# Performance work log

Measured on AMD Instinct MI355X. Metric: run time of the kernel, lower is better.

Reference implementation:

```python
import jax, jax.numpy as jnp
import numpy as np

B, C, T = 2, 128, 25000
OUT_C = 128
N_NODES = B * T            # 50000, nodes after flatten
N_EDGES = 800000           # avg degree 16


def setup_inputs() -> dict:
    key = jax.random.key(0)
    k1, k2, k3 = jax.random.split(key, 3)
    x = jax.random.normal(k1, (B, C, T), dtype=jnp.float32)
    W = jax.random.normal(k2, (C, OUT_C), dtype=jnp.float32) * (1.0 / np.sqrt(C))
    bias = jnp.zeros((OUT_C,), dtype=jnp.float32)
    edge_index = jax.random.randint(k3, (2, N_EDGES), 0, N_NODES, dtype=jnp.int64)
    return {"x": x, "W": W, "bias": bias, "edge_index": edge_index}


def reference(x, W, bias, edge_index):
    b, c, t = x.shape
    n = b * t
    flat = x.transpose(0, 2, 1).reshape(n, c)          # [N, C]
    h = flat @ W                                       # [N, OUT_C] transform first (GCNConv)
    src, dst = edge_index[0], edge_index[1]
    # in-degree with self-loops (PyG GCNConv default symmetric norm)
    deg = jnp.zeros((n,), dtype=h.dtype).at[dst].add(1.0) + 1.0
    dinv_sqrt = jax.lax.rsqrt(deg)
    norm = dinv_sqrt[src] * dinv_sqrt[dst]             # [E]
    msgs = h[src] * norm[:, None]                      # [E, OUT_C] gather + scale
    agg = jax.ops.segment_sum(msgs, dst, num_segments=n)
    agg = agg + h * (1.0 / deg)[:, None]               # self-loop term: norm_ii = 1/deg_i
    out = jax.nn.relu(agg + bias)
    return out.reshape(b, t, -1).transpose(0, 2, 1)    # [B, OUT_C, T]
```

## Files before the change

kernel.cpp:

```cpp
#include <hip/hip_runtime.h>

#define TT 25000
#define BB 2
#define CC 128
#define NN (BB*TT)
#define NB ((NN + 255) / 256)

typedef __attribute__((ext_vector_type(8))) short bf16x8;
typedef __attribute__((ext_vector_type(4))) float f32x4;

__device__ inline unsigned short f2bf(float f) {
    unsigned int u = __float_as_uint(f);
    u += 0x7FFF + ((u >> 16) & 1);
    return (unsigned short)(u >> 16);
}
__device__ inline float bfhi(unsigned int v) { return __uint_as_float(v << 16); }
__device__ inline float bflo(unsigned int v) { return __uint_as_float(v & 0xFFFF0000u); }

__global__ __launch_bounds__(256) void k_deg(const int* __restrict__ dst, int E,
                                             int* __restrict__ deg,
                                             int* __restrict__ eseq) {
    int base = blockIdx.x * 1024 + threadIdx.x;
    int d[4]; bool ok[4];
#pragma unroll
    for (int u = 0; u < 4; ++u) {
        int i = base + u * 256;
        ok[u] = (i < E);
        d[u] = ok[u] ? dst[i] : 0;
    }
#pragma unroll
    for (int u = 0; u < 4; ++u)
        if (ok[u]) eseq[base + u * 256] = atomicAdd(&deg[d[u]], 1);
}

__global__ __launch_bounds__(256) void k_bsum(const int* __restrict__ deg,
                                              int* __restrict__ bsum) {
    __shared__ int red[256];
    int tid = threadIdx.x;
    int i = blockIdx.x * 256 + tid;
    red[tid] = (i < NN) ? deg[i] : 0;
    __syncthreads();
#pragma unroll
    for (int o = 128; o > 0; o >>= 1) {
        if (tid < o) red[tid] += red[tid + o];
        __syncthreads();
    }
    if (tid == 0) bsum[blockIdx.x] = red[0];
}

__global__ __launch_bounds__(256) void k_scan2(const int* __restrict__ deg,
                                               const int* __restrict__ bsum,
                                               int* __restrict__ off,
                                               float* __restrict__ dinv) {
    __shared__ int part[256];
    __shared__ int bpref;
    int tid = threadIdx.x;
    int i = blockIdx.x * 256 + tid;

    part[tid] = (tid < NB && tid < blockIdx.x) ? bsum[tid] : 0;
    __syncthreads();
#pragma unroll
    for (int o = 128; o > 0; o >>= 1) {
        if (tid < o) part[tid] += part[tid + o];
        __syncthreads();
    }
    if (tid == 0) bpref = part[0];
    __syncthreads();
    int base = bpref;
    __syncthreads();

    int v = (i < NN) ? deg[i] : 0;
    part[tid] = v;
    __syncthreads();
#pragma unroll
    for (int o = 1; o < 256; o <<= 1) {
        int u = (tid >= o) ? part[tid - o] : 0;
        __syncthreads();
        part[tid] += u;
        __syncthreads();
    }
    int incl = part[tid];
    if (i < NN) {
        off[i]  = base + incl - v;
        dinv[i] = rsqrtf((float)(v + 1));
    }
    if (i == NN - 1) off[NN] = base + incl;
}

__global__ __launch_bounds__(256) void k_fill(const int* __restrict__ src,
                                              const int* __restrict__ dst, int E,
                                              const int* __restrict__ off,
                                              const int* __restrict__ eseq,
                                              int* __restrict__ csr_src) {
    int i = blockIdx.x * blockDim.x + threadIdx.x;
    if (i < E) {
        int d = dst[i];
        csr_src[off[d] + eseq[i]] = src[i];
    }
}

__global__ __launch_bounds__(256) void k_gemm(const float* __restrict__ x,
                                              const float* __restrict__ W,
                                              const float* __restrict__ dinv,
                                              unsigned short* __restrict__ h) {
    __shared__ __align__(16) unsigned short a_lds[4][4][64][8];
    __shared__ __align__(16) unsigned short b_lds[8][4][64][8];
    int tid = threadIdx.x;
    int n0 = blockIdx.x * 64;

    {
        int m = tid & 63;
        int n = n0 + m;
        bool ok = (n < NN);
        int b = 0, t = 0;
        if (ok) { b = n / TT; t = n - b * TT; }
        const float* xp = x + ((size_t)b * CC) * TT + t;
        int mt = m >> 4, lm = m & 15;
#pragma unroll
        for (int p = 0; p < 4; ++p) {
            int kg = (tid >> 6) + p * 4;
            unsigned short tmp[8];
#pragma unroll
            for (int j = 0; j < 8; ++j) {
                float v = ok ? xp[(size_t)(kg * 8 + j) * TT] : 0.f;
                tmp[j] = f2bf(v);
            }
            int kk = kg >> 2, q = kg & 3;
            *(bf16x8*)&a_lds[mt][kk][lm | (q << 4)][0] = *(bf16x8*)tmp;
        }
    }
    {
        int nc = tid & 127;
        int nt = nc >> 4, ln = nc & 15;
#pragma unroll
        for (int p = 0; p < 8; ++p) {
            int kg = (tid >> 7) + p * 2;
            unsigned short tmp[8];
#pragma unroll
            for (int j = 0; j < 8; ++j)
                tmp[j] = f2bf(W[(kg * 8 + j) * CC + nc]);
            int kk = kg >> 2, q = kg & 3;
            *(bf16x8*)&b_lds[nt][kk][ln | (q << 4)][0] = *(bf16x8*)tmp;
        }
    }
    __syncthreads();

    int lane = tid & 63;
    int w = tid >> 6;
    f32x4 acc[8];
#pragma unroll
    for (int nt = 0; nt < 8; ++nt) acc[nt] = (f32x4){0.f, 0.f, 0.f, 0.f};
#pragma unroll
    for (int kk = 0; kk < 4; ++kk) {
        bf16x8 a = *(const bf16x8*)&a_lds[w][kk][lane][0];
#pragma unroll
        for (int nt = 0; nt < 8; ++nt) {
            bf16x8 bb = *(const bf16x8*)&b_lds[nt][kk][lane][0];
            acc[nt] = __builtin_amdgcn_mfma_f32_16x16x32_bf16(a, bb, acc[nt], 0, 0, 0);
        }
    }

    int q = lane >> 4, col = lane & 15;
    int nodebase = n0 + w * 16 + q * 4;
    float di[4];
#pragma unroll
    for (int r = 0; r < 4; ++r) {
        int nn = nodebase + r;
        di[r] = (nn < NN) ? dinv[nn] : 0.f;
    }
#pragma unroll
    for (int nt = 0; nt < 8; ++nt) {
#pragma unroll
        for (int r = 0; r < 4; ++r) {
            int nn = nodebase + r;
            if (nn < NN)
                h[(size_t)nn * CC + nt * 16 + col] = f2bf(di[r] * acc[nt][r]);
        }
    }
}

__global__ __launch_bounds__(256) void k_agg(const unsigned int* __restrict__ hb,
                                             const int* __restrict__ off,
                                             const int* __restrict__ csr_src,
                                             const float* __restrict__ dinv,
                                             const float* __restrict__ bias,
                                             unsigned int* __restrict__ agg16) {
    int lane = threadIdx.x & 63;
    int w    = threadIdx.x >> 6;
    int n    = blockIdx.x * 4 + w;
    if (n >= NN) return;
    float ax = 0.f, ay = 0.f;
    int e0 = off[n], e1 = off[n + 1];

    for (int c0 = e0; c0 < e1; c0 += 64) {
        int cnt = e1 - c0; if (cnt > 64) cnt = 64;
        int li = lane < cnt ? lane : cnt - 1;
        int iv = csr_src[c0 + li];
        int j = 0;
        for (; j + 16 <= cnt; j += 16) {
            int s[16];
#pragma unroll
            for (int u = 0; u < 16; ++u) s[u] = __shfl(iv, j + u, 64);
            unsigned int v[16];
#pragma unroll
            for (int u = 0; u < 16; ++u) v[u] = hb[(size_t)s[u] * 64 + lane];
#pragma unroll
            for (int u = 0; u < 16; ++u) { ax += bfhi(v[u]); ay += bflo(v[u]); }
        }
        for (; j + 4 <= cnt; j += 4) {
            int s[4];
#pragma unroll
            for (int u = 0; u < 4; ++u) s[u] = __shfl(iv, j + u, 64);
            unsigned int v[4];
#pragma unroll
            for (int u = 0; u < 4; ++u) v[u] = hb[(size_t)s[u] * 64 + lane];
#pragma unroll
            for (int u = 0; u < 4; ++u) { ax += bfhi(v[u]); ay += bflo(v[u]); }
        }
        for (; j < cnt; ++j) {
            int s = __shfl(iv, j, 64);
            unsigned int v = hb[(size_t)s * 64 + lane];
            ax += bfhi(v); ay += bflo(v);
        }
    }

    unsigned int hv = hb[(size_t)n * 64 + lane];
    ax += bfhi(hv);
    ay += bflo(hv);
    float di = dinv[n];
    const float2* b2 = (const float2*)bias;
    float2 bb = b2[lane];
    float rx = fmaxf(fmaf(di, ax, bb.x), 0.f);
    float ry = fmaxf(fmaf(di, ay, bb.y), 0.f);
    unsigned int packed = (unsigned int)f2bf(rx) | ((unsigned int)f2bf(ry) << 16);
    agg16[(size_t)n * 64 + lane] = packed;
}

__global__ void k_trans(const unsigned int* __restrict__ agg16, float* __restrict__ out) {
    __shared__ float tile[32][65];
    int t0 = blockIdx.x * 32;
    int p0 = blockIdx.y * 32;
    int b  = blockIdx.z;
    int tx = threadIdx.x, ty = threadIdx.y;
#pragma unroll
    for (int i = 0; i < 4; ++i) {
        int t = t0 + ty + i * 8;
        if (t < TT) {
            unsigned int u = agg16[(size_t)(b * TT + t) * 64 + p0 + tx];
            tile[ty + i * 8][2 * tx]     = bfhi(u);
            tile[ty + i * 8][2 * tx + 1] = bflo(u);
        }
    }
    __syncthreads();
    int t = t0 + tx;
    if (t < TT) {
#pragma unroll
        for (int i = 0; i < 8; ++i) {
            int ch = ty + i * 8;
            out[((size_t)b * CC + 2 * p0 + ch) * TT + t] = tile[tx][ch];
        }
    }
}

extern "C" void kernel_launch(void* const* d_in, const int* in_sizes, int n_in,
                              void* d_out, int out_size, void* d_ws, size_t ws_size,
                              hipStream_t stream) {
    const float* x    = (const float*)d_in[0];
    const float* W    = (const float*)d_in[1];
    const float* bias = (const float*)d_in[2];
    const int*   ei   = (const int*)d_in[3];
    int E = in_sizes[3] / 2;
    const int* src = ei;
    const int* dst = ei + E;
    float* out = (float*)d_out;

    char* ws = (char*)d_ws;
    size_t o = 0;
    unsigned short* h = (unsigned short*)(ws + o); o += (size_t)NN * CC * 2;
    unsigned int* agg16 = (unsigned int*)(ws + o); o += (size_t)NN * 64 * 4;
    int*   deg  = (int*)  (ws + o); o += (size_t)NN * 4;
    float* dinv = (float*)(ws + o); o += (size_t)NN * 4;
    int*   off  = (int*)  (ws + o); o += (size_t)(NN + 1) * 4 + 12;
    int*   bsum = (int*)  (ws + o); o += (size_t)((NB + 3) & ~3) * 4;
    int*   eseq = (int*)  (ws + o); o += (size_t)E * 4;
    int*   csrs = (int*)  (ws + o); o += (size_t)E * 4;

    hipMemsetAsync(deg, 0, (size_t)NN * 4, stream);

    k_deg  <<<(E + 1023) / 1024, 256, 0, stream>>>(dst, E, deg, eseq);
    k_bsum <<<NB, 256, 0, stream>>>(deg, bsum);
    k_scan2<<<NB, 256, 0, stream>>>(deg, bsum, off, dinv);
    k_fill <<<(E + 255) / 256, 256, 0, stream>>>(src, dst, E, off, eseq, csrs);
    k_gemm <<<(NN + 63) / 64, 256, 0, stream>>>(x, W, dinv, h);
    k_agg  <<<(NN + 3) / 4, 256, 0, stream>>>((const unsigned int*)h, off, csrs, dinv, bias, agg16);
    dim3 tg((TT + 31) / 32, 2, BB);
    k_trans<<<tg, dim3(32, 8), 0, stream>>>(agg16, out);
}
```

Measured before the change: 191.0 us.

## Use 16-bit CSR indices and gather two edges per wave in aggregation

CSR source indices and per-edge sequence numbers are stored as 16-bit values, which relies on the node count (50000) and per-node in-degree fitting below 65536; this halves the index traffic in the fill and aggregation kernels. The aggregation kernel now splits each wave into two half-waves. Each half-wave gathers a different edge's 256-byte row using 8-byte loads, and a final cross-half shuffle reduction combines the two partial sums. This doubles the gathers in flight per instruction but adds a reduction step and a masked tail for an odd edge count.

```diff
diff --git a/kernel.cpp b/kernel.cpp
--- a/kernel.cpp
+++ b/kernel.cpp
@@ -19,7 +19,7 @@
 
 __global__ __launch_bounds__(256) void k_deg(const int* __restrict__ dst, int E,
                                              int* __restrict__ deg,
-                                             int* __restrict__ eseq) {
+                                             unsigned short* __restrict__ eseq) {
     int base = blockIdx.x * 1024 + threadIdx.x;
     int d[4]; bool ok[4];
 #pragma unroll
@@ -30,7 +30,7 @@
     }
 #pragma unroll
     for (int u = 0; u < 4; ++u)
-        if (ok[u]) eseq[base + u * 256] = atomicAdd(&deg[d[u]], 1);
+        if (ok[u]) eseq[base + u * 256] = (unsigned short)atomicAdd(&deg[d[u]], 1);
 }
 
 __global__ __launch_bounds__(256) void k_bsum(const int* __restrict__ deg,
@@ -90,12 +90,12 @@
 __global__ __launch_bounds__(256) void k_fill(const int* __restrict__ src,
                                               const int* __restrict__ dst, int E,
                                               const int* __restrict__ off,
-                                              const int* __restrict__ eseq,
-                                              int* __restrict__ csr_src) {
+                                              const unsigned short* __restrict__ eseq,
+                                              unsigned short* __restrict__ csr16) {
     int i = blockIdx.x * blockDim.x + threadIdx.x;
     if (i < E) {
         int d = dst[i];
-        csr_src[off[d] + eseq[i]] = src[i];
+        csr16[off[d] + (int)eseq[i]] = (unsigned short)src[i];
     }
 }
 
@@ -179,61 +179,87 @@
     }
 }
 
-__global__ __launch_bounds__(256) void k_agg(const unsigned int* __restrict__ hb,
+__global__ __launch_bounds__(256) void k_agg(const uint2* __restrict__ hb2,
                                              const int* __restrict__ off,
-                                             const int* __restrict__ csr_src,
+                                             const unsigned short* __restrict__ csr16,
                                              const float* __restrict__ dinv,
                                              const float* __restrict__ bias,
-                                             unsigned int* __restrict__ agg16) {
+                                             uint2* __restrict__ agg16) {
     int lane = threadIdx.x & 63;
     int w    = threadIdx.x >> 6;
     int n    = blockIdx.x * 4 + w;
     if (n >= NN) return;
-    float ax = 0.f, ay = 0.f;
+    int sub = lane & 31;
+    int ep  = lane >> 5;
+    float a0 = 0.f, a1 = 0.f, a2 = 0.f, a3 = 0.f;
     int e0 = off[n], e1 = off[n + 1];
 
     for (int c0 = e0; c0 < e1; c0 += 64) {
         int cnt = e1 - c0; if (cnt > 64) cnt = 64;
         int li = lane < cnt ? lane : cnt - 1;
-        int iv = csr_src[c0 + li];
+        int iv = (int)csr16[c0 + li];
         int j = 0;
-        for (; j + 16 <= cnt; j += 16) {
+        for (; j + 32 <= cnt; j += 32) {
             int s[16];
 #pragma unroll
-            for (int u = 0; u < 16; ++u) s[u] = __shfl(iv, j + u, 64);
-            unsigned int v[16];
-#pragma unroll
-            for (int u = 0; u < 16; ++u) v[u] = hb[(size_t)s[u] * 64 + lane];
-#pragma unroll
-            for (int u = 0; u < 16; ++u) { ax += bfhi(v[u]); ay += bflo(v[u]); }
-        }
-        for (; j + 4 <= cnt; j += 4) {
+            for (int u = 0; u < 16; ++u) s[u] = __shfl(iv, j + 2 * u + ep, 64);
+            uint2 v[16];
+#pragma unroll
+            for (int u = 0; u < 16; ++u) v[u] = hb2[(size_t)s[u] * 32 + sub];
+#pragma unroll
+            for (int u = 0; u < 16; ++u) {
+                a0 += bfhi(v[u].x); a1 += bflo(v[u].x);
+                a2 += bfhi(v[u].y); a3 += bflo(v[u].y);
+            }
+        }
+        for (; j + 8 <= cnt; j += 8) {
             int s[4];
 #pragma unroll
-            for (int u = 0; u < 4; ++u) s[u] = __shfl(iv, j + u, 64);
-            unsigned int v[4];
-#pragma unroll
-            for (int u = 0; u < 4; ++u) v[u] = hb[(size_t)s[u] * 64 + lane];
-#pragma unroll
-            for (int u = 0; u < 4; ++u) { ax += bfhi(v[u]); ay += bflo(v[u]); }
-        }
-        for (; j < cnt; ++j) {
+            for (int u = 0; u < 4; ++u) s[u] = __shfl(iv, j + 2 * u + ep, 64);
+            uint2 v[4];
+#pragma unroll
+            for (int u = 0; u < 4; ++u) v[u] = hb2[(size_t)s[u] * 32 + sub];
+#pragma unroll
+            for (int u = 0; u < 4; ++u) {
+                a0 += bfhi(v[u].x); a1 += bflo(v[u].x);
+                a2 += bfhi(v[u].y); a3 += bflo(v[u].y);
+            }
+        }
+        for (; j + 2 <= cnt; j += 2) {
+            int s = __shfl(iv, j + ep, 64);
+            uint2 v = hb2[(size_t)s * 32 + sub];
+            a0 += bfhi(v.x); a1 += bflo(v.x);
+            a2 += bfhi(v.y); a3 += bflo(v.y);
+        }
+        if (j < cnt) {
             int s = __shfl(iv, j, 64);
-            unsigned int v = hb[(size_t)s * 64 + lane];
-            ax += bfhi(v); ay += bflo(v);
-        }
-    }
-
-    unsigned int hv = hb[(size_t)n * 64 + lane];
-    ax += bfhi(hv);
-    ay += bflo(hv);
-    float di = dinv[n];
-    const float2* b2 = (const float2*)bias;
-    float2 bb = b2[lane];
-    float rx = fmaxf(fmaf(di, ax, bb.x), 0.f);
-    float ry = fmaxf(fmaf(di, ay, bb.y), 0.f);
-    unsigned int packed = (unsigned int)f2bf(rx) | ((unsigned int)f2bf(ry) << 16);
-    agg16[(size_t)n * 64 + lane] = packed;
+            uint2 v = hb2[(size_t)s * 32 + sub];
+            if (ep == 0) {
+                a0 += bfhi(v.x); a1 += bflo(v.x);
+                a2 += bfhi(v.y); a3 += bflo(v.y);
+            }
+        }
+    }
+    a0 += __shfl_xor(a0, 32, 64);
+    a1 += __shfl_xor(a1, 32, 64);
+    a2 += __shfl_xor(a2, 32, 64);
+    a3 += __shfl_xor(a3, 32, 64);
+
+    if (ep == 0) {
+        uint2 hv = hb2[(size_t)n * 32 + sub];
+        a0 += bfhi(hv.x); a1 += bflo(hv.x);
+        a2 += bfhi(hv.y); a3 += bflo(hv.y);
+        float di = dinv[n];
+        float4 bb = ((const float4*)bias)[sub];
+        float r0 = fmaxf(fmaf(di, a0, bb.x), 0.f);
+        float r1 = fmaxf(fmaf(di, a1, bb.y), 0.f);
+        float r2 = fmaxf(fmaf(di, a2, bb.z), 0.f);
+        float r3 = fmaxf(fmaf(di, a3, bb.w), 0.f);
+        uint2 pk;
+        pk.x = (unsigned int)f2bf(r0) | ((unsigned int)f2bf(r1) << 16);
+        pk.y = (unsigned int)f2bf(r2) | ((unsigned int)f2bf(r3) << 16);
+        agg16[(size_t)n * 32 + sub] = pk;
+    }
 }
 
 __global__ void k_trans(const unsigned int* __restrict__ agg16, float* __restrict__ out) {
@@ -282,17 +308,17 @@
     float* dinv = (float*)(ws + o); o += (size_t)NN * 4;
     int*   off  = (int*)  (ws + o); o += (size_t)(NN + 1) * 4 + 12;
     int*   bsum = (int*)  (ws + o); o += (size_t)((NB + 3) & ~3) * 4;
-    int*   eseq = (int*)  (ws + o); o += (size_t)E * 4;
-    int*   csrs = (int*)  (ws + o); o += (size_t)E * 4;
+    unsigned short* eseq  = (unsigned short*)(ws + o); o += (size_t)E * 2;
+    unsigned short* csr16 = (unsigned short*)(ws + o); o += (size_t)E * 2;
 
     hipMemsetAsync(deg, 0, (size_t)NN * 4, stream);
 
     k_deg  <<<(E + 1023) / 1024, 256, 0, stream>>>(dst, E, deg, eseq);
     k_bsum <<<NB, 256, 0, stream>>>(deg, bsum);
     k_scan2<<<NB, 256, 0, stream>>>(deg, bsum, off, dinv);
-    k_fill <<<(E + 255) / 256, 256, 0, stream>>>(src, dst, E, off, eseq, csrs);
+    k_fill <<<(E + 255) / 256, 256, 0, stream>>>(src, dst, E, off, eseq, csr16);
     k_gemm <<<(NN + 63) / 64, 256, 0, stream>>>(x, W, dinv, h);
-    k_agg  <<<(NN + 3) / 4, 256, 0, stream>>>((const unsigned int*)h, off, csrs, dinv, bias, agg16);
+    k_agg  <<<(NN + 3) / 4, 256, 0, stream>>>((const uint2*)h, off, csr16, dinv, bias, (uint2*)agg16);
     dim3 tg((TT + 31) / 32, 2, BB);
     k_trans<<<tg, dim3(32, 8), 0, stream>>>(agg16, out);
 }
```

Result: no change. 191.7 us (+0.4%).
